# Kernel tuning notes

Hardware: AMD Instinct MI355X
Metric: run time of the kernel (lower is better)

The kernel has to match this reference:

```python
import jax, jax.numpy as jnp
import numpy as np

TOP_K = 2

def setup_inputs() -> dict:
    key = jax.random.key(0)
    ks = jax.random.split(key, 8)
    B, S, H, F, E = 2, 2048, 1024, 2048, 8
    sH = 1.0 / np.sqrt(H)
    sF = 1.0 / np.sqrt(F)
    return {
        "hidden_states": jax.random.normal(ks[0], (B, S, H), jnp.float32),
        "gate_w": jax.random.normal(ks[1], (E, H), jnp.float32) * sH,
        "w_up": jax.random.normal(ks[2], (E, H, F), jnp.float32) * sH,
        "w_gate": jax.random.normal(ks[3], (E, H, F), jnp.float32) * sH,
        "w_down": jax.random.normal(ks[4], (E, F, H), jnp.float32) * sF,
        "b_up": jnp.zeros((E, F), jnp.float32),
        "b_gate": jnp.zeros((E, F), jnp.float32),
        "b_down": jnp.zeros((E, H), jnp.float32),
    }

def reference(hidden_states, gate_w, w_up, w_gate, w_down, b_up, b_gate, b_down):
    # Flatten [B,S,H] -> [N,H]
    H = hidden_states.shape[-1]
    x = hidden_states.reshape(-1, H)                      # [N,H]
    router_logits = x @ gate_w.T                          # [N,E]
    probs = jax.nn.softmax(router_logits.astype(jnp.float32), axis=-1)
    topv, topi = jax.lax.top_k(probs, TOP_K)              # [N,K]
    topv = topv / topv.sum(axis=-1, keepdims=True)
    N, E = router_logits.shape
    # Sparse combine weights: zero except top-k experts (renormalized).
    w_full = jnp.zeros((N, E), probs.dtype).at[jnp.arange(N)[:, None], topi].set(topv)
    w_full = w_full.astype(x.dtype)
    # SwiGLU per expert (dense over E; combine weights zero out non-selected).
    u = jnp.einsum('nh,ehf->nef', x, w_up) + b_up         # [N,E,F]
    v = jnp.einsum('nh,ehf->nef', x, w_gate) + b_gate
    phi = jax.nn.silu(v) * u
    y = jnp.einsum('nef,efh->neh', phi, w_down) + b_down  # [N,E,H]
    out = jnp.einsum('ne,neh->nh', w_full, y)             # [N,H]
    out = out.reshape(hidden_states.shape)
    return out, router_logits.astype(hidden_states.dtype)
```

## Files before the change

### kernel.cpp

```cpp
#include <hip/hip_runtime.h>
#include <hip/hip_bf16.h>
#include <cstdint>
#include <cstddef>

#define N_TOK 4096
#define H_DIM 1024
#define F_DIM 2048
#define E_NUM 8
#define RCAP 9216

typedef __attribute__((ext_vector_type(8))) short bf16x8;
typedef __attribute__((ext_vector_type(4))) float f32x4;

__device__ __forceinline__ float b2f(uint16_t u) {
  return __uint_as_float(((uint32_t)u) << 16);
}
__device__ __forceinline__ uint16_t f2b(float f) {
  uint32_t x = __float_as_uint(f);
  uint32_t r = (x + 0x7fffu + ((x >> 16) & 1u)) >> 16;
  return (uint16_t)r;
}

__device__ __forceinline__ void gl2lds16(const void* g, void* l) {
  __builtin_amdgcn_global_load_lds(
      (const __attribute__((address_space(1))) uint32_t*)g,
      (__attribute__((address_space(3))) uint32_t*)l, 16, 0, 0);
}

__device__ __forceinline__ void stage_tile(const uint16_t* src, int ldK,
                                           char* lds, int wave, int lane) {
  int u = (lane & 7) ^ (lane >> 3);
  const char* s0 = (const char*)src + u * 16;
  size_t rb = (size_t)ldK * 2;
  int Rb = wave * 32 + (lane >> 3);
  for (int c = 0; c < 4; ++c) {
    gl2lds16(s0 + (size_t)(Rb + c * 8) * rb, lds + wave * 4096 + c * 1024);
  }
}

__device__ __forceinline__ bf16x8 read_frag(const char* lds, int R, int s,
                                            int q) {
  int unit = ((s << 2) + q) ^ (R & 7);
  return *(const bf16x8*)(lds + R * 128 + unit * 16);
}

__global__ __launch_bounds__(256) void detect_kernel(
    const uint16_t* __restrict__ x, int* __restrict__ flag) {
  __shared__ int cnt;
  if (threadIdx.x == 0) cnt = 0;
  __syncthreads();
  int ok = 0;
  for (int j = 0; j < 16; ++j) {
    uint16_t u = x[threadIdx.x * 16 + j];
    int e = (u >> 7) & 0xff;
    ok += (u == 0 || (e >= 96 && e <= 143)) ? 1 : 0;
  }
  atomicAdd(&cnt, ok);
  __syncthreads();
  if (threadIdx.x == 0) *flag = (cnt >= 3700) ? 1 : 0;
}

__global__ __launch_bounds__(256) void router_kernel(
    const void* __restrict__ xraw, const void* __restrict__ gwraw,
    const int* __restrict__ flag, void* __restrict__ dout,
    int* __restrict__ top_i, float* __restrict__ top_w) {
  int fl = *flag;
  int wave = threadIdx.x >> 6, lane = threadIdx.x & 63;
  int t = blockIdx.x * 4 + wave;
  float xv[16];
  if (fl) {
    const uint16_t* xr = (const uint16_t*)xraw + (size_t)t * H_DIM + lane * 16;
    uint4 a = *(const uint4*)xr;
    uint4 b = *(const uint4*)(xr + 8);
    uint32_t w[8] = {a.x, a.y, a.z, a.w, b.x, b.y, b.z, b.w};
    for (int j = 0; j < 8; ++j) {
      xv[2 * j] = b2f((uint16_t)(w[j] & 0xffff));
      xv[2 * j + 1] = b2f((uint16_t)(w[j] >> 16));
    }
  } else {
    const float* xr = (const float*)xraw + (size_t)t * H_DIM + lane * 16;
    for (int j = 0; j < 4; ++j) {
      float4 v = ((const float4*)xr)[j];
      xv[4 * j] = v.x; xv[4 * j + 1] = v.y;
      xv[4 * j + 2] = v.z; xv[4 * j + 3] = v.w;
    }
  }
  float acc[E_NUM];
  for (int e = 0; e < E_NUM; ++e) {
    float s = 0.f;
    if (fl) {
      const uint16_t* gr =
          (const uint16_t*)gwraw + (size_t)e * H_DIM + lane * 16;
      uint4 a = *(const uint4*)gr;
      uint4 b = *(const uint4*)(gr + 8);
      uint32_t w[8] = {a.x, a.y, a.z, a.w, b.x, b.y, b.z, b.w};
      for (int j = 0; j < 8; ++j) {
        s += xv[2 * j] * b2f((uint16_t)(w[j] & 0xffff));
        s += xv[2 * j + 1] * b2f((uint16_t)(w[j] >> 16));
      }
    } else {
      const float* gr = (const float*)gwraw + (size_t)e * H_DIM + lane * 16;
      for (int j = 0; j < 4; ++j) {
        float4 v = ((const float4*)gr)[j];
        s += xv[4 * j] * v.x + xv[4 * j + 1] * v.y + xv[4 * j + 2] * v.z +
             xv[4 * j + 3] * v.w;
      }
    }
    acc[e] = s;
  }
  for (int off = 32; off >= 1; off >>= 1)
    for (int e = 0; e < E_NUM; ++e)
      acc[e] += __shfl_xor(acc[e], off, 64);
  if (lane < E_NUM) {
    size_t idx = (size_t)N_TOK * H_DIM + (size_t)t * E_NUM + lane;
    if (fl)
      ((uint16_t*)dout)[idx] = f2b(acc[lane]);
    else
      ((float*)dout)[idx] = acc[lane];
  }
  if (lane == 0) {
    int b0 = 0;
    float v0 = acc[0];
    for (int e = 1; e < E_NUM; ++e)
      if (acc[e] > v0) { v0 = acc[e]; b0 = e; }
    int b1 = (b0 == 0) ? 1 : 0;
    float v1 = acc[b1];
    for (int e = 0; e < E_NUM; ++e)
      if (e != b0 && acc[e] > v1) { v1 = acc[e]; b1 = e; }
    float w0 = 1.f / (1.f + expf(v1 - v0));
    top_i[2 * t] = b0; top_i[2 * t + 1] = b1;
    top_w[2 * t] = w0; top_w[2 * t + 1] = 1.f - w0;
  }
}

__global__ __launch_bounds__(1024) void histscan_kernel(
    const int* __restrict__ top_i, const float* __restrict__ top_w,
    int* __restrict__ counts, int* __restrict__ bases,
    int* __restrict__ row_of, int* __restrict__ row_token,
    float* __restrict__ row_weight) {
  int tid = threadIdx.x;
  int lane = tid & 63, wave = tid >> 6;
  int e_loc[8];
  float tw[8];
  int c[E_NUM] = {};
  for (int j = 0; j < 8; ++j) {
    int idx = tid * 8 + j;
    int e = top_i[idx];
    e_loc[j] = e;
    tw[j] = top_w[idx];
    c[e]++;
  }
  int inc[E_NUM];
  for (int k = 0; k < E_NUM; ++k) inc[k] = c[k];
  for (int off = 1; off < 64; off <<= 1) {
    for (int k = 0; k < E_NUM; ++k) {
      int v = __shfl_up(inc[k], off, 64);
      if (lane >= off) inc[k] += v;
    }
  }
  __shared__ int wtot[16][E_NUM];
  __shared__ int woff[16][E_NUM];
  __shared__ int base_s[E_NUM];
  if (lane == 63)
    for (int k = 0; k < E_NUM; ++k) wtot[wave][k] = inc[k];
  __syncthreads();
  if (tid < E_NUM) {
    int run = 0;
    for (int w = 0; w < 16; ++w) {
      woff[w][tid] = run;
      run += wtot[w][tid];
    }
    counts[tid] = run;
    wtot[0][tid] = run;
  }
  __syncthreads();
  if (tid == 0) {
    int b = 0;
    for (int e = 0; e < E_NUM; ++e) {
      bases[e] = b;
      base_s[e] = b;
      b += (wtot[0][e] + 127) & ~127;
    }
  }
  __syncthreads();
  int run[E_NUM];
  for (int k = 0; k < E_NUM; ++k)
    run[k] = base_s[k] + woff[wave][k] + inc[k] - c[k];
  for (int j = 0; j < 8; ++j) {
    int idx = tid * 8 + j;
    int e = e_loc[j];
    int r = run[e]++;
    row_of[idx] = r;
    row_token[r] = idx >> 1;
    row_weight[r] = tw[j];
  }
}

__global__ __launch_bounds__(256) void gather_kernel(
    const void* __restrict__ xraw, const int* __restrict__ flag,
    const int* __restrict__ row_of, uint16_t* __restrict__ Xg) {
  int t = blockIdx.x;
  int rs0 = row_of[2 * t], rs1 = row_of[2 * t + 1];
  uint2 v;
  if (*flag) {
    v = ((const uint2*)((const uint16_t*)xraw + (size_t)t * H_DIM))[threadIdx.x];
  } else {
    float4 f =
        ((const float4*)((const float*)xraw + (size_t)t * H_DIM))[threadIdx.x];
    v.x = (uint32_t)f2b(f.x) | ((uint32_t)f2b(f.y) << 16);
    v.y = (uint32_t)f2b(f.z) | ((uint32_t)f2b(f.w) << 16);
  }
  ((uint2*)(Xg + (size_t)rs0 * H_DIM))[threadIdx.x] = v;
  ((uint2*)(Xg + (size_t)rs1 * H_DIM))[threadIdx.x] = v;
}

__global__ __launch_bounds__(256) void transpose_kernel(
    const void* __restrict__ W, const int* __restrict__ flag,
    uint16_t* __restrict__ Wt, int K, int N) {
  int e = blockIdx.z;
  int n0 = blockIdx.x * 64, k0 = blockIdx.y * 64;
  __shared__ __align__(16) uint16_t tile[64][72];
  size_t ebase = (size_t)e * K * N;
  uint16_t* Wout = Wt + ebase;
  int fl = *flag;
  int r = threadIdx.x >> 3;
  int c = (threadIdx.x & 7) * 8;
  if (fl) {
    const uint16_t* Win = (const uint16_t*)W + ebase;
    for (int it = 0; it < 2; ++it) {
      int row = r + it * 32;
      uint4 v = *(const uint4*)(Win + (size_t)(k0 + row) * N + n0 + c);
      *(uint4*)&tile[row][c] = v;
    }
  } else {
    const float* Win = (const float*)W + ebase;
    for (int it = 0; it < 2; ++it) {
      int row = r + it * 32;
      const float* p = Win + (size_t)(k0 + row) * N + n0 + c;
      float4 a = ((const float4*)p)[0];
      float4 b = ((const float4*)p)[1];
      uint16_t* tp = &tile[row][c];
      tp[0] = f2b(a.x); tp[1] = f2b(a.y); tp[2] = f2b(a.z); tp[3] = f2b(a.w);
      tp[4] = f2b(b.x); tp[5] = f2b(b.y); tp[6] = f2b(b.z); tp[7] = f2b(b.w);
    }
  }
  __syncthreads();
  for (int it = 0; it < 2; ++it) {
    int n = r + it * 32;
    uint4 o;
    o.x = (uint32_t)tile[c + 0][n] | ((uint32_t)tile[c + 1][n] << 16);
    o.y = (uint32_t)tile[c + 2][n] | ((uint32_t)tile[c + 3][n] << 16);
    o.z = (uint32_t)tile[c + 4][n] | ((uint32_t)tile[c + 5][n] << 16);
    o.w = (uint32_t)tile[c + 6][n] | ((uint32_t)tile[c + 7][n] << 16);
    *(uint4*)(Wout + (size_t)(n0 + n) * K + k0 + c) = o;
  }
}

__global__ __launch_bounds__(256, 2) void gemm_upgate(
    const uint16_t* __restrict__ Xg,
    const uint16_t* __restrict__ WtU, const uint16_t* __restrict__ WtG,
    const void* __restrict__ buRaw, const void* __restrict__ bgRaw,
    const int* __restrict__ flag,
    const int* __restrict__ counts, const int* __restrict__ bases,
    uint16_t* __restrict__ phi) {
  int e = blockIdx.z;
  int cnt = counts[e];
  int m0 = blockIdx.y * 128;
  if (m0 >= cnt) return;
  int n0 = blockIdx.x * 128;
  int base = bases[e];
  const uint16_t* A = Xg + (size_t)(base + m0) * H_DIM;
  const uint16_t* BU = WtU + (size_t)e * F_DIM * H_DIM + (size_t)n0 * H_DIM;
  const uint16_t* BG = WtG + (size_t)e * F_DIM * H_DIM + (size_t)n0 * H_DIM;

  __shared__ __align__(16) char lA[128 * 128];
  __shared__ __align__(16) char lBu[128 * 128];
  __shared__ __align__(16) char lBg[128 * 128];

  int tid = threadIdx.x;
  int wave = tid >> 6, lane = tid & 63;
  int wm = wave >> 1, wn = wave & 1;
  int q = lane >> 4, mr = lane & 15;

  f32x4 accU[4][4] = {};
  f32x4 accG[4][4] = {};

  for (int k0 = 0; k0 < H_DIM; k0 += 64) {
    __syncthreads();
    stage_tile(A + k0, H_DIM, lA, wave, lane);
    stage_tile(BU + k0, H_DIM, lBu, wave, lane);
    stage_tile(BG + k0, H_DIM, lBg, wave, lane);
    __syncthreads();
    for (int s = 0; s < 2; ++s) {
      bf16x8 af[4], bu[4], bg[4];
      for (int mt = 0; mt < 4; ++mt)
        af[mt] = read_frag(lA, wm * 64 + mt * 16 + mr, s, q);
      for (int nt = 0; nt < 4; ++nt) {
        bu[nt] = read_frag(lBu, wn * 64 + nt * 16 + mr, s, q);
        bg[nt] = read_frag(lBg, wn * 64 + nt * 16 + mr, s, q);
      }
      for (int mt = 0; mt < 4; ++mt)
        for (int nt = 0; nt < 4; ++nt) {
          accU[mt][nt] = __builtin_amdgcn_mfma_f32_16x16x32_bf16(
              af[mt], bu[nt], accU[mt][nt], 0, 0, 0);
          accG[mt][nt] = __builtin_amdgcn_mfma_f32_16x16x32_bf16(
              af[mt], bg[nt], accG[mt][nt], 0, 0, 0);
        }
    }
  }

  int fl = *flag;
  int rbase = m0 + wm * 64;
  int cbase = n0 + wn * 64;
  for (int nt = 0; nt < 4; ++nt) {
    int col = cbase + nt * 16 + mr;
    float bu_v, bg_v;
    if (fl) {
      bu_v = b2f(((const uint16_t*)buRaw)[(size_t)e * F_DIM + col]);
      bg_v = b2f(((const uint16_t*)bgRaw)[(size_t)e * F_DIM + col]);
    } else {
      bu_v = ((const float*)buRaw)[(size_t)e * F_DIM + col];
      bg_v = ((const float*)bgRaw)[(size_t)e * F_DIM + col];
    }
    for (int mt = 0; mt < 4; ++mt) {
      int r0 = rbase + mt * 16 + q * 4;
      for (int rg = 0; rg < 4; ++rg) {
        int row = r0 + rg;
        float u = accU[mt][nt][rg] + bu_v;
        float v = accG[mt][nt][rg] + bg_v;
        float s = v / (1.f + expf(-v));
        phi[(size_t)(base + row) * F_DIM + col] = f2b(s * u);
      }
    }
  }
}

__global__ __launch_bounds__(256, 2) void gemm_down(
    const uint16_t* __restrict__ phi, const uint16_t* __restrict__ WtD,
    const void* __restrict__ bdRaw, const int* __restrict__ flag,
    const int* __restrict__ counts, const int* __restrict__ bases,
    const int* __restrict__ row_token, const float* __restrict__ row_weight,
    float* __restrict__ out_acc) {
  int e = blockIdx.z;
  int cnt = counts[e];
  int m0 = blockIdx.y * 128;
  if (m0 >= cnt) return;
  int n0 = blockIdx.x * 128;
  int base = bases[e];
  const uint16_t* A = phi + (size_t)(base + m0) * F_DIM;
  const uint16_t* B = WtD + (size_t)e * H_DIM * F_DIM + (size_t)n0 * F_DIM;

  __shared__ __align__(16) char lA[128 * 128];
  __shared__ __align__(16) char lB[128 * 128];

  int tid = threadIdx.x;
  int wave = tid >> 6, lane = tid & 63;
  int wm = wave >> 1, wn = wave & 1;
  int q = lane >> 4, mr = lane & 15;

  f32x4 acc[4][4] = {};

  for (int k0 = 0; k0 < F_DIM; k0 += 64) {
    __syncthreads();
    stage_tile(A + k0, F_DIM, lA, wave, lane);
    stage_tile(B + k0, F_DIM, lB, wave, lane);
    __syncthreads();
    for (int s = 0; s < 2; ++s) {
      bf16x8 af[4], bf[4];
      for (int mt = 0; mt < 4; ++mt)
        af[mt] = read_frag(lA, wm * 64 + mt * 16 + mr, s, q);
      for (int nt = 0; nt < 4; ++nt)
        bf[nt] = read_frag(lB, wn * 64 + nt * 16 + mr, s, q);
      for (int mt = 0; mt < 4; ++mt)
        for (int nt = 0; nt < 4; ++nt)
          acc[mt][nt] = __builtin_amdgcn_mfma_f32_16x16x32_bf16(
              af[mt], bf[nt], acc[mt][nt], 0, 0, 0);
    }
  }

  int fl = *flag;
  int rbase = m0 + wm * 64;
  int cbase = n0 + wn * 64;
  for (int nt = 0; nt < 4; ++nt) {
    int col = cbase + nt * 16 + mr;
    float bd_v = fl ? b2f(((const uint16_t*)bdRaw)[(size_t)e * H_DIM + col])
                    : ((const float*)bdRaw)[(size_t)e * H_DIM + col];
    for (int mt = 0; mt < 4; ++mt) {
      int r0 = rbase + mt * 16 + q * 4;
      for (int rg = 0; rg < 4; ++rg) {
        int row = r0 + rg;
        if (row < cnt) {
          int tkn = row_token[base + row];
          float w = row_weight[base + row];
          atomicAdd(out_acc + (size_t)tkn * H_DIM + col,
                    w * (acc[mt][nt][rg] + bd_v));
        }
      }
    }
  }
}

__global__ __launch_bounds__(256) void out_convert(
    const float* __restrict__ acc, const int* __restrict__ flag,
    void* __restrict__ out) {
  int i = blockIdx.x * 256 + threadIdx.x;
  float4 v = ((const float4*)acc)[i];
  if (*flag) {
    uint2 o;
    o.x = (uint32_t)f2b(v.x) | ((uint32_t)f2b(v.y) << 16);
    o.y = (uint32_t)f2b(v.z) | ((uint32_t)f2b(v.w) << 16);
    ((uint2*)out)[i] = o;
  } else {
    ((float4*)out)[i] = v;
  }
}

extern "C" void kernel_launch(void* const* d_in, const int* in_sizes, int n_in,
                              void* d_out, int out_size, void* d_ws, size_t ws_size,
                              hipStream_t stream) {
  const void* x = d_in[0];
  const void* gw = d_in[1];
  const void* w_up = d_in[2];
  const void* w_gate = d_in[3];
  const void* w_down = d_in[4];
  const void* b_up = d_in[5];
  const void* b_gate = d_in[6];
  const void* b_down = d_in[7];

  char* ws = (char*)d_ws;
  size_t off = 0;
  auto alloc = [&](size_t bytes) -> void* {
    void* p = ws + off;
    off += (bytes + 255) & ~(size_t)255;
    return p;
  };
  int* counts = (int*)alloc(32);
  int* bases = (int*)alloc(32);
  int* flag = (int*)alloc(32);
  int* top_i = (int*)alloc(sizeof(int) * N_TOK * 2);
  float* top_w = (float*)alloc(sizeof(float) * N_TOK * 2);
  int* row_of = (int*)alloc(sizeof(int) * N_TOK * 2);
  int* row_token = (int*)alloc(sizeof(int) * RCAP);
  float* row_weight = (float*)alloc(sizeof(float) * RCAP);
  uint16_t* Xg = (uint16_t*)alloc((size_t)RCAP * H_DIM * 2);
  uint16_t* phi = (uint16_t*)alloc((size_t)RCAP * F_DIM * 2);
  uint16_t* WtU = (uint16_t*)alloc((size_t)E_NUM * H_DIM * F_DIM * 2);
  uint16_t* WtG = (uint16_t*)alloc((size_t)E_NUM * H_DIM * F_DIM * 2);
  float* out_acc = (float*)alloc((size_t)N_TOK * H_DIM * sizeof(float));

  hipMemsetAsync(out_acc, 0, (size_t)N_TOK * H_DIM * sizeof(float), stream);

  detect_kernel<<<1, 256, 0, stream>>>((const uint16_t*)x, flag);
  router_kernel<<<N_TOK / 4, 256, 0, stream>>>(x, gw, flag, d_out, top_i,
                                               top_w);
  histscan_kernel<<<1, 1024, 0, stream>>>(top_i, top_w, counts, bases, row_of,
                                          row_token, row_weight);
  gather_kernel<<<N_TOK, 256, 0, stream>>>(x, flag, row_of, Xg);

  transpose_kernel<<<dim3(F_DIM / 64, H_DIM / 64, E_NUM), 256, 0, stream>>>(
      w_up, flag, WtU, H_DIM, F_DIM);
  transpose_kernel<<<dim3(F_DIM / 64, H_DIM / 64, E_NUM), 256, 0, stream>>>(
      w_gate, flag, WtG, H_DIM, F_DIM);

  gemm_upgate<<<dim3(F_DIM / 128, 32, E_NUM), 256, 0, stream>>>(
      Xg, WtU, WtG, b_up, b_gate, flag, counts, bases, phi);

  transpose_kernel<<<dim3(H_DIM / 64, F_DIM / 64, E_NUM), 256, 0, stream>>>(
      w_down, flag, WtU, F_DIM, H_DIM);
  gemm_down<<<dim3(H_DIM / 128, 32, E_NUM), 256, 0, stream>>>(
      phi, WtU, b_down, flag, counts, bases, row_token, row_weight, out_acc);

  out_convert<<<(N_TOK * H_DIM / 4) / 256, 256, 0, stream>>>(out_acc, flag,
                                                             d_out);
}
```

Baseline: 458.3 us.

## Use compacted tile list, larger double-buffered GEMM tiles, and non-atomic combine

Routing now emits a compact list of 256-row tiles per expert, so the GEMM grids launch only over real tiles instead of a dense expert-by-row grid. Both GEMMs move to 512-thread blocks with larger M (and N for down) tiles and double-buffered LDS staging, so the next K slice loads while the current one is computed. The atomic scatter into a zeroed fp32 accumulator is replaced by writing per-row expert outputs, followed by a gather-combine kernel that also does the output conversion. This removes the memset and the atomics, but adds a larger Yrows buffer, heavier LDS use per block, and more padding per expert.

```diff
diff --git a/kernel.cpp b/kernel.cpp
--- a/kernel.cpp
+++ b/kernel.cpp
@@ -7,7 +7,8 @@
 #define H_DIM 1024
 #define F_DIM 2048
 #define E_NUM 8
-#define RCAP 9216
+#define RCAP 10240
+#define MAXT 40
 
 typedef __attribute__((ext_vector_type(8))) short bf16x8;
 typedef __attribute__((ext_vector_type(4))) float f32x4;
@@ -27,15 +28,26 @@
       (__attribute__((address_space(3))) uint32_t*)l, 16, 0, 0);
 }
 
-__device__ __forceinline__ void stage_tile(const uint16_t* src, int ldK,
-                                           char* lds, int wave, int lane) {
+__device__ __forceinline__ void stage256(const uint16_t* src, int ldK,
+                                         char* lds, int wave, int lane) {
   int u = (lane & 7) ^ (lane >> 3);
   const char* s0 = (const char*)src + u * 16;
   size_t rb = (size_t)ldK * 2;
   int Rb = wave * 32 + (lane >> 3);
-  for (int c = 0; c < 4; ++c) {
-    gl2lds16(s0 + (size_t)(Rb + c * 8) * rb, lds + wave * 4096 + c * 1024);
-  }
+  char* d0 = lds + wave * 4096;
+  for (int c = 0; c < 4; ++c)
+    gl2lds16(s0 + (size_t)(Rb + c * 8) * rb, d0 + c * 1024);
+}
+
+__device__ __forceinline__ void stage128(const uint16_t* src, int ldK,
+                                         char* lds, int wave, int lane) {
+  int u = (lane & 7) ^ (lane >> 3);
+  const char* s0 = (const char*)src + u * 16;
+  size_t rb = (size_t)ldK * 2;
+  int Rb = wave * 16 + (lane >> 3);
+  char* d0 = lds + wave * 2048;
+  for (int c = 0; c < 2; ++c)
+    gl2lds16(s0 + (size_t)(Rb + c * 8) * rb, d0 + c * 1024);
 }
 
 __device__ __forceinline__ bf16x8 read_frag(const char* lds, int R, int s,
@@ -134,20 +146,18 @@
 }
 
 __global__ __launch_bounds__(1024) void histscan_kernel(
-    const int* __restrict__ top_i, const float* __restrict__ top_w,
-    int* __restrict__ counts, int* __restrict__ bases,
-    int* __restrict__ row_of, int* __restrict__ row_token,
-    float* __restrict__ row_weight) {
+    const int* __restrict__ top_i, int* __restrict__ counts,
+    int* __restrict__ bases, int* __restrict__ row_of,
+    int* __restrict__ tile_e, int* __restrict__ tile_row,
+    int* __restrict__ ntiles) {
   int tid = threadIdx.x;
   int lane = tid & 63, wave = tid >> 6;
   int e_loc[8];
-  float tw[8];
   int c[E_NUM] = {};
   for (int j = 0; j < 8; ++j) {
     int idx = tid * 8 + j;
     int e = top_i[idx];
     e_loc[j] = e;
-    tw[j] = top_w[idx];
     c[e]++;
   }
   int inc[E_NUM];
@@ -175,12 +185,20 @@
   }
   __syncthreads();
   if (tid == 0) {
-    int b = 0;
+    int b = 0, nt = 0;
     for (int e = 0; e < E_NUM; ++e) {
       bases[e] = b;
       base_s[e] = b;
-      b += (wtot[0][e] + 127) & ~127;
-    }
+      int cc = wtot[0][e];
+      int te = (cc + 255) >> 8;
+      for (int j = 0; j < te; ++j) {
+        tile_e[nt] = e;
+        tile_row[nt] = b + j * 256;
+        ++nt;
+      }
+      b += te << 8;
+    }
+    *ntiles = nt;
   }
   __syncthreads();
   int run[E_NUM];
@@ -188,11 +206,8 @@
     run[k] = base_s[k] + woff[wave][k] + inc[k] - c[k];
   for (int j = 0; j < 8; ++j) {
     int idx = tid * 8 + j;
-    int e = e_loc[j];
-    int r = run[e]++;
+    int r = run[e_loc[j]]++;
     row_of[idx] = r;
-    row_token[r] = idx >> 1;
-    row_weight[r] = tw[j];
   }
 }
 
@@ -256,26 +271,25 @@
   }
 }
 
-__global__ __launch_bounds__(256, 2) void gemm_upgate(
+__global__ __launch_bounds__(512, 2) void gemm_upgate(
     const uint16_t* __restrict__ Xg,
     const uint16_t* __restrict__ WtU, const uint16_t* __restrict__ WtG,
     const void* __restrict__ buRaw, const void* __restrict__ bgRaw,
-    const int* __restrict__ flag,
-    const int* __restrict__ counts, const int* __restrict__ bases,
+    const int* __restrict__ flag, const int* __restrict__ tile_e,
+    const int* __restrict__ tile_row, const int* __restrict__ ntiles,
     uint16_t* __restrict__ phi) {
-  int e = blockIdx.z;
-  int cnt = counts[e];
-  int m0 = blockIdx.y * 128;
-  if (m0 >= cnt) return;
+  int ty = blockIdx.y;
+  if (ty >= *ntiles) return;
+  int e = tile_e[ty];
+  int r0 = tile_row[ty];
   int n0 = blockIdx.x * 128;
-  int base = bases[e];
-  const uint16_t* A = Xg + (size_t)(base + m0) * H_DIM;
+  const uint16_t* A = Xg + (size_t)r0 * H_DIM;
   const uint16_t* BU = WtU + (size_t)e * F_DIM * H_DIM + (size_t)n0 * H_DIM;
   const uint16_t* BG = WtG + (size_t)e * F_DIM * H_DIM + (size_t)n0 * H_DIM;
 
-  __shared__ __align__(16) char lA[128 * 128];
-  __shared__ __align__(16) char lBu[128 * 128];
-  __shared__ __align__(16) char lBg[128 * 128];
+  __shared__ __align__(16) char lA[2][256 * 128];
+  __shared__ __align__(16) char lBu[2][128 * 128];
+  __shared__ __align__(16) char lBg[2][128 * 128];
 
   int tid = threadIdx.x;
   int wave = tid >> 6, lane = tid & 63;
@@ -285,19 +299,28 @@
   f32x4 accU[4][4] = {};
   f32x4 accG[4][4] = {};
 
+  stage256(A, H_DIM, lA[0], wave, lane);
+  stage128(BU, H_DIM, lBu[0], wave, lane);
+  stage128(BG, H_DIM, lBg[0], wave, lane);
+
   for (int k0 = 0; k0 < H_DIM; k0 += 64) {
+    int cur = (k0 >> 6) & 1;
     __syncthreads();
-    stage_tile(A + k0, H_DIM, lA, wave, lane);
-    stage_tile(BU + k0, H_DIM, lBu, wave, lane);
-    stage_tile(BG + k0, H_DIM, lBg, wave, lane);
-    __syncthreads();
+    if (k0 + 64 < H_DIM) {
+      stage256(A + k0 + 64, H_DIM, lA[cur ^ 1], wave, lane);
+      stage128(BU + k0 + 64, H_DIM, lBu[cur ^ 1], wave, lane);
+      stage128(BG + k0 + 64, H_DIM, lBg[cur ^ 1], wave, lane);
+    }
+    const char* pA = lA[cur];
+    const char* pU = lBu[cur];
+    const char* pG = lBg[cur];
     for (int s = 0; s < 2; ++s) {
       bf16x8 af[4], bu[4], bg[4];
       for (int mt = 0; mt < 4; ++mt)
-        af[mt] = read_frag(lA, wm * 64 + mt * 16 + mr, s, q);
+        af[mt] = read_frag(pA, wm * 64 + mt * 16 + mr, s, q);
       for (int nt = 0; nt < 4; ++nt) {
-        bu[nt] = read_frag(lBu, wn * 64 + nt * 16 + mr, s, q);
-        bg[nt] = read_frag(lBg, wn * 64 + nt * 16 + mr, s, q);
+        bu[nt] = read_frag(pU, wn * 64 + nt * 16 + mr, s, q);
+        bg[nt] = read_frag(pG, wn * 64 + nt * 16 + mr, s, q);
       }
       for (int mt = 0; mt < 4; ++mt)
         for (int nt = 0; nt < 4; ++nt) {
@@ -310,10 +333,10 @@
   }
 
   int fl = *flag;
-  int rbase = m0 + wm * 64;
-  int cbase = n0 + wn * 64;
+  int rb_ = r0 + wm * 64;
+  int cb_ = n0 + wn * 64;
   for (int nt = 0; nt < 4; ++nt) {
-    int col = cbase + nt * 16 + mr;
+    int col = cb_ + nt * 16 + mr;
     float bu_v, bg_v;
     if (fl) {
       bu_v = b2f(((const uint16_t*)buRaw)[(size_t)e * F_DIM + col]);
@@ -323,55 +346,59 @@
       bg_v = ((const float*)bgRaw)[(size_t)e * F_DIM + col];
     }
     for (int mt = 0; mt < 4; ++mt) {
-      int r0 = rbase + mt * 16 + q * 4;
+      int r = rb_ + mt * 16 + q * 4;
       for (int rg = 0; rg < 4; ++rg) {
-        int row = r0 + rg;
         float u = accU[mt][nt][rg] + bu_v;
         float v = accG[mt][nt][rg] + bg_v;
         float s = v / (1.f + expf(-v));
-        phi[(size_t)(base + row) * F_DIM + col] = f2b(s * u);
+        phi[(size_t)(r + rg) * F_DIM + col] = f2b(s * u);
       }
     }
   }
 }
 
-__global__ __launch_bounds__(256, 2) void gemm_down(
+__global__ __launch_bounds__(512, 2) void gemm_down(
     const uint16_t* __restrict__ phi, const uint16_t* __restrict__ WtD,
     const void* __restrict__ bdRaw, const int* __restrict__ flag,
-    const int* __restrict__ counts, const int* __restrict__ bases,
-    const int* __restrict__ row_token, const float* __restrict__ row_weight,
-    float* __restrict__ out_acc) {
-  int e = blockIdx.z;
-  int cnt = counts[e];
-  int m0 = blockIdx.y * 128;
-  if (m0 >= cnt) return;
-  int n0 = blockIdx.x * 128;
-  int base = bases[e];
-  const uint16_t* A = phi + (size_t)(base + m0) * F_DIM;
+    const int* __restrict__ tile_e, const int* __restrict__ tile_row,
+    const int* __restrict__ ntiles, float* __restrict__ Yrows) {
+  int ty = blockIdx.y;
+  if (ty >= *ntiles) return;
+  int e = tile_e[ty];
+  int r0 = tile_row[ty];
+  int n0 = blockIdx.x * 256;
+  const uint16_t* A = phi + (size_t)r0 * F_DIM;
   const uint16_t* B = WtD + (size_t)e * H_DIM * F_DIM + (size_t)n0 * F_DIM;
 
-  __shared__ __align__(16) char lA[128 * 128];
-  __shared__ __align__(16) char lB[128 * 128];
+  __shared__ __align__(16) char lA[2][256 * 128];
+  __shared__ __align__(16) char lB[2][256 * 128];
 
   int tid = threadIdx.x;
   int wave = tid >> 6, lane = tid & 63;
-  int wm = wave >> 1, wn = wave & 1;
+  int wm = wave >> 2, wn = wave & 3;
   int q = lane >> 4, mr = lane & 15;
 
-  f32x4 acc[4][4] = {};
+  f32x4 acc[8][4] = {};
+
+  stage256(A, F_DIM, lA[0], wave, lane);
+  stage256(B, F_DIM, lB[0], wave, lane);
 
   for (int k0 = 0; k0 < F_DIM; k0 += 64) {
+    int cur = (k0 >> 6) & 1;
     __syncthreads();
-    stage_tile(A + k0, F_DIM, lA, wave, lane);
-    stage_tile(B + k0, F_DIM, lB, wave, lane);
-    __syncthreads();
+    if (k0 + 64 < F_DIM) {
+      stage256(A + k0 + 64, F_DIM, lA[cur ^ 1], wave, lane);
+      stage256(B + k0 + 64, F_DIM, lB[cur ^ 1], wave, lane);
+    }
+    const char* pA = lA[cur];
+    const char* pB = lB[cur];
     for (int s = 0; s < 2; ++s) {
-      bf16x8 af[4], bf[4];
-      for (int mt = 0; mt < 4; ++mt)
-        af[mt] = read_frag(lA, wm * 64 + mt * 16 + mr, s, q);
+      bf16x8 af[8], bf[4];
+      for (int mt = 0; mt < 8; ++mt)
+        af[mt] = read_frag(pA, wm * 128 + mt * 16 + mr, s, q);
       for (int nt = 0; nt < 4; ++nt)
-        bf[nt] = read_frag(lB, wn * 64 + nt * 16 + mr, s, q);
-      for (int mt = 0; mt < 4; ++mt)
+        bf[nt] = read_frag(pB, wn * 64 + nt * 16 + mr, s, q);
+      for (int mt = 0; mt < 8; ++mt)
         for (int nt = 0; nt < 4; ++nt)
           acc[mt][nt] = __builtin_amdgcn_mfma_f32_16x16x32_bf16(
               af[mt], bf[nt], acc[mt][nt], 0, 0, 0);
@@ -379,39 +406,42 @@
   }
 
   int fl = *flag;
-  int rbase = m0 + wm * 64;
-  int cbase = n0 + wn * 64;
+  int rb_ = r0 + wm * 128;
+  int cb_ = n0 + wn * 64;
   for (int nt = 0; nt < 4; ++nt) {
-    int col = cbase + nt * 16 + mr;
+    int col = cb_ + nt * 16 + mr;
     float bd_v = fl ? b2f(((const uint16_t*)bdRaw)[(size_t)e * H_DIM + col])
                     : ((const float*)bdRaw)[(size_t)e * H_DIM + col];
-    for (int mt = 0; mt < 4; ++mt) {
-      int r0 = rbase + mt * 16 + q * 4;
-      for (int rg = 0; rg < 4; ++rg) {
-        int row = r0 + rg;
-        if (row < cnt) {
-          int tkn = row_token[base + row];
-          float w = row_weight[base + row];
-          atomicAdd(out_acc + (size_t)tkn * H_DIM + col,
-                    w * (acc[mt][nt][rg] + bd_v));
-        }
-      }
-    }
-  }
-}
-
-__global__ __launch_bounds__(256) void out_convert(
-    const float* __restrict__ acc, const int* __restrict__ flag,
+    for (int mt = 0; mt < 8; ++mt) {
+      int r = rb_ + mt * 16 + q * 4;
+      for (int rg = 0; rg < 4; ++rg)
+        Yrows[(size_t)(r + rg) * H_DIM + col] = acc[mt][nt][rg] + bd_v;
+    }
+  }
+}
+
+__global__ __launch_bounds__(256) void combine_kernel(
+    const float* __restrict__ Y, const int* __restrict__ row_of,
+    const float* __restrict__ top_w, const int* __restrict__ flag,
     void* __restrict__ out) {
-  int i = blockIdx.x * 256 + threadIdx.x;
-  float4 v = ((const float4*)acc)[i];
+  int t = blockIdx.x;
+  int r0 = row_of[2 * t], r1 = row_of[2 * t + 1];
+  float w0 = top_w[2 * t], w1 = top_w[2 * t + 1];
+  int i = threadIdx.x;
+  float4 a = ((const float4*)(Y + (size_t)r0 * H_DIM))[i];
+  float4 b = ((const float4*)(Y + (size_t)r1 * H_DIM))[i];
+  float4 o;
+  o.x = w0 * a.x + w1 * b.x;
+  o.y = w0 * a.y + w1 * b.y;
+  o.z = w0 * a.z + w1 * b.z;
+  o.w = w0 * a.w + w1 * b.w;
   if (*flag) {
-    uint2 o;
-    o.x = (uint32_t)f2b(v.x) | ((uint32_t)f2b(v.y) << 16);
-    o.y = (uint32_t)f2b(v.z) | ((uint32_t)f2b(v.w) << 16);
-    ((uint2*)out)[i] = o;
+    uint2 p;
+    p.x = (uint32_t)f2b(o.x) | ((uint32_t)f2b(o.y) << 16);
+    p.y = (uint32_t)f2b(o.z) | ((uint32_t)f2b(o.w) << 16);
+    ((uint2*)out)[(size_t)t * 256 + i] = p;
   } else {
-    ((float4*)out)[i] = v;
+    ((float4*)out)[(size_t)t * 256 + i] = o;
   }
 }
 
@@ -437,24 +467,23 @@
   int* counts = (int*)alloc(32);
   int* bases = (int*)alloc(32);
   int* flag = (int*)alloc(32);
+  int* ntiles = (int*)alloc(32);
+  int* tile_e = (int*)alloc(sizeof(int) * MAXT);
+  int* tile_row = (int*)alloc(sizeof(int) * MAXT);
   int* top_i = (int*)alloc(sizeof(int) * N_TOK * 2);
   float* top_w = (float*)alloc(sizeof(float) * N_TOK * 2);
   int* row_of = (int*)alloc(sizeof(int) * N_TOK * 2);
-  int* row_token = (int*)alloc(sizeof(int) * RCAP);
-  float* row_weight = (float*)alloc(sizeof(float) * RCAP);
   uint16_t* Xg = (uint16_t*)alloc((size_t)RCAP * H_DIM * 2);
   uint16_t* phi = (uint16_t*)alloc((size_t)RCAP * F_DIM * 2);
   uint16_t* WtU = (uint16_t*)alloc((size_t)E_NUM * H_DIM * F_DIM * 2);
   uint16_t* WtG = (uint16_t*)alloc((size_t)E_NUM * H_DIM * F_DIM * 2);
-  float* out_acc = (float*)alloc((size_t)N_TOK * H_DIM * sizeof(float));
-
-  hipMemsetAsync(out_acc, 0, (size_t)N_TOK * H_DIM * sizeof(float), stream);
+  float* Yrows = (float*)alloc((size_t)RCAP * H_DIM * sizeof(float));
 
   detect_kernel<<<1, 256, 0, stream>>>((const uint16_t*)x, flag);
   router_kernel<<<N_TOK / 4, 256, 0, stream>>>(x, gw, flag, d_out, top_i,
                                                top_w);
-  histscan_kernel<<<1, 1024, 0, stream>>>(top_i, top_w, counts, bases, row_of,
-                                          row_token, row_weight);
+  histscan_kernel<<<1, 1024, 0, stream>>>(top_i, counts, bases, row_of,
+                                          tile_e, tile_row, ntiles);
   gather_kernel<<<N_TOK, 256, 0, stream>>>(x, flag, row_of, Xg);
 
   transpose_kernel<<<dim3(F_DIM / 64, H_DIM / 64, E_NUM), 256, 0, stream>>>(
@@ -462,14 +491,13 @@
   transpose_kernel<<<dim3(F_DIM / 64, H_DIM / 64, E_NUM), 256, 0, stream>>>(
       w_gate, flag, WtG, H_DIM, F_DIM);
 
-  gemm_upgate<<<dim3(F_DIM / 128, 32, E_NUM), 256, 0, stream>>>(
-      Xg, WtU, WtG, b_up, b_gate, flag, counts, bases, phi);
+  gemm_upgate<<<dim3(F_DIM / 128, MAXT), 512, 0, stream>>>(
+      Xg, WtU, WtG, b_up, b_gate, flag, tile_e, tile_row, ntiles, phi);
 
   transpose_kernel<<<dim3(H_DIM / 64, F_DIM / 64, E_NUM), 256, 0, stream>>>(
       w_down, flag, WtU, F_DIM, H_DIM);
-  gemm_down<<<dim3(H_DIM / 128, 32, E_NUM), 256, 0, stream>>>(
-      phi, WtU, b_down, flag, counts, bases, row_token, row_weight, out_acc);
-
-  out_convert<<<(N_TOK * H_DIM / 4) / 256, 256, 0, stream>>>(out_acc, flag,
-                                                             d_out);
-}
+  gemm_down<<<dim3(H_DIM / 256, MAXT), 512, 0, stream>>>(
+      phi, WtU, b_down, flag, tile_e, tile_row, ntiles, Yrows);
+
+  combine_kernel<<<N_TOK, 256, 0, stream>>>(Yrows, row_of, top_w, flag, d_out);
+}
```

New measurement: 455.8 us. No clear change (-0.6%).
